# Kernel optimization log

Hardware: AMD Instinct MI355X
Metric: run time of the kernel (lower is better)

The kernel has to match this reference:

```python
import jax, jax.numpy as jnp
import numpy as np

K = 7        # kernel_size
G = 16       # group_number
STRIDE = 1
BN_EPS = 1e-5


def setup_inputs() -> dict:
    key = jax.random.key(0)
    ks = jax.random.split(key, 3)
    B, C, H, W = 2, 256, 56, 56
    Cr = C // 4  # reduction_ratio = 4
    x = jax.random.normal(ks[0], (B, C, H, W), dtype=jnp.float32)
    w1 = jax.random.normal(ks[1], (Cr, C), dtype=jnp.float32) * (1.0 / np.sqrt(C))
    b1 = jnp.zeros((Cr,), dtype=jnp.float32)
    gamma = jnp.ones((Cr,), dtype=jnp.float32)
    beta = jnp.zeros((Cr,), dtype=jnp.float32)
    w2 = jax.random.normal(ks[2], (K * K * G, Cr), dtype=jnp.float32) * (1.0 / np.sqrt(Cr))
    b2 = jnp.zeros((K * K * G,), dtype=jnp.float32)
    return {"x": x, "w1": w1, "b1": b1, "gamma": gamma, "beta": beta, "w2": w2, "b2": b2}


def _kernel_gen(x, w1, b1, gamma, beta, w2, b2):
    # 1x1 conv -> BatchNorm (training-mode batch stats) -> ReLU -> 1x1 conv
    t = jnp.einsum('oc,bchw->bohw', w1, x) + b1[None, :, None, None]
    mean = t.mean(axis=(0, 2, 3), keepdims=True)
    var = t.var(axis=(0, 2, 3), keepdims=True)
    t = (t - mean) * jax.lax.rsqrt(var + BN_EPS)
    t = t * gamma[None, :, None, None] + beta[None, :, None, None]
    t = jax.nn.relu(t)
    return jnp.einsum('oc,bchw->bohw', w2, t) + b2[None, :, None, None]


def reference(x, w1, b1, gamma, beta, w2, b2):
    B, C, H, W = x.shape
    nh, nw = H // STRIDE, W // STRIDE  # stride == 1 here
    # kernel generation (stride==1 -> no avg_pool)
    k = _kernel_gen(x, w1, b1, gamma, beta, w2, b2)          # (B, K*K*G, nh, nw)
    kernel = k.reshape(B, K * K, nh, nw, G)                   # raw view, as in torch
    # F.unfold with padding=K//2, stride=1 -> layout (B, C*K*K, L), c-major then k
    p = K // 2
    xp = jnp.pad(x, ((0, 0), (0, 0), (p, p), (p, p)))
    patches = jnp.stack(
        [xp[:, :, i:i + nh, j:j + nw] for i in range(K) for j in range(K)],
        axis=2)                                               # (B, C, K*K, nh, nw)
    flat = patches.reshape(B, C * K * K, nh * nw)             # == torch F.unfold
    ip = flat.reshape(B, C // G, K * K, nh, nw, G)            # raw view, as in torch
    out = (kernel[:, None] * ip).sum(axis=2)                  # (B, C//G, nh, nw, G)
    out = out.reshape(B, C, nh, nw)                           # raw view, as in torch
    return out, kernel
```

## Files before the change

### kernel.cpp

```cpp
#include <hip/hip_runtime.h>

#define HW     3136
#define C_IN   256
#define CR     64
#define KKG    784
#define NB     2
#define NPIX   6272
#define NT25   25
#define BN_EPS 1e-5f

__device__ float g_P[4 * CR * NPIX];
__device__ float g_T[CR * NPIX];
__device__ float g_bs[2 * CR * NT25];
__device__ float g_ss[2 * CR];
__device__ float g_xg[16 * NPIX * 16];

__global__ __launch_bounds__(256) void k1a_conv1(const float* __restrict__ x,
                                                 const float* __restrict__ w1) {
  int p = blockIdx.x * 256 + threadIdx.x;
  if (p >= NPIX) return;
  int o0 = blockIdx.y * 4;
  int kc = blockIdx.z;
  int b  = p / HW;
  int u  = p - b * HW;

  const float* xb = x + ((size_t)(b * C_IN + kc * 64)) * HW + u;
  const float* w  = w1 + kc * 64;

  float a0 = 0.f, a1 = 0.f, a2 = 0.f, a3 = 0.f;
#pragma unroll 8
  for (int c = 0; c < 64; ++c) {
    float xv = xb[(size_t)c * HW];
    a0 += w[(o0 + 0) * C_IN + c] * xv;
    a1 += w[(o0 + 1) * C_IN + c] * xv;
    a2 += w[(o0 + 2) * C_IN + c] * xv;
    a3 += w[(o0 + 3) * C_IN + c] * xv;
  }
  float* pp = g_P + ((size_t)kc * CR + o0) * NPIX + p;
  pp[0 * NPIX] = a0; pp[1 * NPIX] = a1; pp[2 * NPIX] = a2; pp[3 * NPIX] = a3;
}

__global__ __launch_bounds__(256) void k1b_reduce(const float* __restrict__ b1) {
  int p = blockIdx.x * 256 + threadIdx.x;
  int o = blockIdx.y;
  bool valid = (p < NPIX);
  float v = 0.0f;
  if (valid) {
    v = b1[o]
      + g_P[((size_t)0 * CR + o) * NPIX + p]
      + g_P[((size_t)1 * CR + o) * NPIX + p]
      + g_P[((size_t)2 * CR + o) * NPIX + p]
      + g_P[((size_t)3 * CR + o) * NPIX + p];
    g_T[(size_t)o * NPIX + p] = v;
  }
  float s  = valid ? v : 0.0f;
  float s2 = valid ? v * v : 0.0f;
#pragma unroll
  for (int off = 32; off > 0; off >>= 1) {
    s  += __shfl_down(s, off);
    s2 += __shfl_down(s2, off);
  }
  __shared__ float sd[8];
  int lane = threadIdx.x & 63, wid = threadIdx.x >> 6;
  if (lane == 0) { sd[wid] = s; sd[4 + wid] = s2; }
  __syncthreads();
  if (threadIdx.x == 0) {
    g_bs[o * NT25 + blockIdx.x]             = sd[0] + sd[1] + sd[2] + sd[3];
    g_bs[CR * NT25 + o * NT25 + blockIdx.x] = sd[4] + sd[5] + sd[6] + sd[7];
  }
}

__global__ __launch_bounds__(256) void k0t_transpose(const float* __restrict__ x,
                                                     const float* __restrict__ gamma,
                                                     const float* __restrict__ beta) {
  int d = blockIdx.x;
  int p = blockIdx.y * 256 + threadIdx.x;
  if (p < NPIX) {
    int b  = (p >= HW) ? 1 : 0;
    int hw = p - b * HW;
    const float* xp = x + ((size_t)(b * C_IN + d)) * HW + hw;
    float r[16];
#pragma unroll
    for (int cg = 0; cg < 16; ++cg)
      r[cg] = xp[(size_t)cg * (16 * HW)];
    float4* dst = (float4*)(g_xg + (((size_t)d * NPIX + p) << 4));
    dst[0] = make_float4(r[0], r[1], r[2], r[3]);
    dst[1] = make_float4(r[4], r[5], r[6], r[7]);
    dst[2] = make_float4(r[8], r[9], r[10], r[11]);
    dst[3] = make_float4(r[12], r[13], r[14], r[15]);
  }
  if (blockIdx.x == 0 && blockIdx.y == 0 && threadIdx.x < CR) {
    int o = threadIdx.x;
    float S = 0.f, S2 = 0.f;
#pragma unroll
    for (int px = 0; px < NT25; ++px) {
      S  += g_bs[o * NT25 + px];
      S2 += g_bs[CR * NT25 + o * NT25 + px];
    }
    const float invN = 1.0f / (float)NPIX;
    float mean = S * invN;
    float var  = S2 * invN - mean * mean;
    float inv  = rsqrtf(var + BN_EPS);
    float sc   = gamma[o] * inv;
    g_ss[o]      = sc;
    g_ss[CR + o] = beta[o] - mean * sc;
  }
}

__global__ __launch_bounds__(256) void k3_conv2(const float* __restrict__ w2,
                                                const float* __restrict__ b2,
                                                float* __restrict__ kout) {
  __shared__ float ssc[CR], ssh[CR];
  if (threadIdx.x < 2 * CR) {
    float v = g_ss[threadIdx.x];
    if (threadIdx.x < CR) ssc[threadIdx.x] = v; else ssh[threadIdx.x - CR] = v;
  }
  __syncthreads();

  int l  = blockIdx.x * 256 + threadIdx.x;
  if (l >= HW) return;
  int o0 = blockIdx.y * 16;
  int b  = blockIdx.z;

  float acc[16];
#pragma unroll
  for (int i = 0; i < 16; ++i) acc[i] = b2[o0 + i];

  const float* Tb = g_T + (size_t)b * HW + l;
  const float* w  = w2 + (size_t)o0 * CR;
#pragma unroll 4
  for (int c = 0; c < CR; ++c) {
    float tv = Tb[(size_t)c * NPIX];
    tv = fmaxf(tv * ssc[c] + ssh[c], 0.0f);
#pragma unroll
    for (int i = 0; i < 16; ++i)
      acc[i] += w[i * CR + c] * tv;
  }
  float* kb = kout + (size_t)(b * KKG + o0) * HW + l;
#pragma unroll
  for (int i = 0; i < 16; ++i) kb[(size_t)i * HW] = acc[i];
}

__global__ __launch_bounds__(256) void k4_invol(const float* __restrict__ kout,
                                                float* __restrict__ out) {
  int base = blockIdx.x * 256 + threadIdx.x;
  int b    = blockIdx.y;
  int cg0  = blockIdx.z * 8;

  int s = base / HW;
  int u = base - s * HW;
  int yrow = u / 56;
  int yy0 = yrow - 3;
  int xx0 = (u - yrow * 56) - 3;

  const float* kb = kout + (size_t)b * (KKG * HW) + base;

  float acc[8];
#pragma unroll
  for (int i = 0; i < 8; ++i) acc[i] = 0.0f;

#pragma unroll 7
  for (int kk = 0; kk < 49; ++kk) {
    int t16 = 16 * kk + s;
    int d   = t16 / 49;
    int kkp = t16 - d * 49;
    int ki  = kkp / 7;
    int kj  = kkp - ki * 7;
    int yy = yy0 + ki, xx = xx0 + kj;
    float kv = kb[(size_t)kk * 50176];
    int off;
    if ((unsigned)yy < 56u && (unsigned)xx < 56u) {
      off = yy * 56 + xx;
    } else {
      off = 0;
      kv = 0.0f;
    }
    const float* xp = g_xg + ((((size_t)d * NPIX + b * HW + off) << 4) + cg0);
    float4 xa = *(const float4*)xp;
    float4 xb4 = *(const float4*)(xp + 4);
    acc[0] += kv * xa.x;  acc[1] += kv * xa.y;
    acc[2] += kv * xa.z;  acc[3] += kv * xa.w;
    acc[4] += kv * xb4.x; acc[5] += kv * xb4.y;
    acc[6] += kv * xb4.z; acc[7] += kv * xb4.w;
  }

  float* ob = out + (size_t)b * (C_IN * HW) + (size_t)cg0 * 50176 + base;
#pragma unroll
  for (int cg = 0; cg < 8; ++cg) ob[(size_t)cg * 50176] = acc[cg];
}

extern "C" void kernel_launch(void* const* d_in, const int* in_sizes, int n_in,
                              void* d_out, int out_size, void* d_ws, size_t ws_size,
                              hipStream_t stream) {
  const float* x     = (const float*)d_in[0];
  const float* w1    = (const float*)d_in[1];
  const float* b1    = (const float*)d_in[2];
  const float* gamma = (const float*)d_in[3];
  const float* beta  = (const float*)d_in[4];
  const float* w2    = (const float*)d_in[5];
  const float* b2    = (const float*)d_in[6];

  float* out  = (float*)d_out;
  float* kout = out + (size_t)NB * C_IN * HW;

  k1a_conv1<<<dim3(25, 16, 4), 256, 0, stream>>>(x, w1);
  k1b_reduce<<<dim3(25, CR), 256, 0, stream>>>(b1);
  k0t_transpose<<<dim3(16, NT25), 256, 0, stream>>>(x, gamma, beta);
  k3_conv2<<<dim3(13, 49, NB), 256, 0, stream>>>(w2, b2, kout);
  k4_invol<<<dim3(196, NB, 2), 256, 0, stream>>>(kout, out);
}
```

Measured before the change: 141.4 us.

## Merge reduce and transpose kernels, fold BN finalize into conv2, regrid involution

Merges the bias-sum/statistics reduction and the x transpose into one launch that picks its role from blockIdx.y. The BN scale/shift finalization moves into every conv2 block, so the g_ss global round trip and the serial single-block step go away. The involution kernel is regridded so each block row maps to one s slice (13x16x4 grid), which removes per-thread division and pads 3136 up to 3328 threads per slice. Together these cut one kernel launch, though every conv2 block now recomputes the BN statistics redundantly.

```diff
diff --git a/kernel.cpp b/kernel.cpp
--- a/kernel.cpp
+++ b/kernel.cpp
@@ -12,7 +12,6 @@
 __device__ float g_P[4 * CR * NPIX];
 __device__ float g_T[CR * NPIX];
 __device__ float g_bs[2 * CR * NT25];
-__device__ float g_ss[2 * CR];
 __device__ float g_xg[16 * NPIX * 16];
 
 __global__ __launch_bounds__(256) void k1a_conv1(const float* __restrict__ x,
@@ -40,42 +39,39 @@
   pp[0 * NPIX] = a0; pp[1 * NPIX] = a1; pp[2 * NPIX] = a2; pp[3 * NPIX] = a3;
 }
 
-__global__ __launch_bounds__(256) void k1b_reduce(const float* __restrict__ b1) {
+__global__ __launch_bounds__(256) void kRT(const float* __restrict__ x,
+                                           const float* __restrict__ b1) {
   int p = blockIdx.x * 256 + threadIdx.x;
-  int o = blockIdx.y;
-  bool valid = (p < NPIX);
-  float v = 0.0f;
-  if (valid) {
-    v = b1[o]
-      + g_P[((size_t)0 * CR + o) * NPIX + p]
-      + g_P[((size_t)1 * CR + o) * NPIX + p]
-      + g_P[((size_t)2 * CR + o) * NPIX + p]
-      + g_P[((size_t)3 * CR + o) * NPIX + p];
-    g_T[(size_t)o * NPIX + p] = v;
-  }
-  float s  = valid ? v : 0.0f;
-  float s2 = valid ? v * v : 0.0f;
-#pragma unroll
-  for (int off = 32; off > 0; off >>= 1) {
-    s  += __shfl_down(s, off);
-    s2 += __shfl_down(s2, off);
-  }
-  __shared__ float sd[8];
-  int lane = threadIdx.x & 63, wid = threadIdx.x >> 6;
-  if (lane == 0) { sd[wid] = s; sd[4 + wid] = s2; }
-  __syncthreads();
-  if (threadIdx.x == 0) {
-    g_bs[o * NT25 + blockIdx.x]             = sd[0] + sd[1] + sd[2] + sd[3];
-    g_bs[CR * NT25 + o * NT25 + blockIdx.x] = sd[4] + sd[5] + sd[6] + sd[7];
-  }
-}
-
-__global__ __launch_bounds__(256) void k0t_transpose(const float* __restrict__ x,
-                                                     const float* __restrict__ gamma,
-                                                     const float* __restrict__ beta) {
-  int d = blockIdx.x;
-  int p = blockIdx.y * 256 + threadIdx.x;
-  if (p < NPIX) {
+  if (blockIdx.y < 64) {
+    int o = blockIdx.y;
+    bool valid = (p < NPIX);
+    float v = 0.0f;
+    if (valid) {
+      v = b1[o]
+        + g_P[((size_t)0 * CR + o) * NPIX + p]
+        + g_P[((size_t)1 * CR + o) * NPIX + p]
+        + g_P[((size_t)2 * CR + o) * NPIX + p]
+        + g_P[((size_t)3 * CR + o) * NPIX + p];
+      g_T[(size_t)o * NPIX + p] = v;
+    }
+    float s  = valid ? v : 0.0f;
+    float s2 = valid ? v * v : 0.0f;
+#pragma unroll
+    for (int off = 32; off > 0; off >>= 1) {
+      s  += __shfl_down(s, off);
+      s2 += __shfl_down(s2, off);
+    }
+    __shared__ float sd[8];
+    int lane = threadIdx.x & 63, wid = threadIdx.x >> 6;
+    if (lane == 0) { sd[wid] = s; sd[4 + wid] = s2; }
+    __syncthreads();
+    if (threadIdx.x == 0) {
+      g_bs[o * NT25 + blockIdx.x]             = sd[0] + sd[1] + sd[2] + sd[3];
+      g_bs[CR * NT25 + o * NT25 + blockIdx.x] = sd[4] + sd[5] + sd[6] + sd[7];
+    }
+  } else {
+    int d = blockIdx.y - 64;
+    if (p >= NPIX) return;
     int b  = (p >= HW) ? 1 : 0;
     int hw = p - b * HW;
     const float* xp = x + ((size_t)(b * C_IN + d)) * HW + hw;
@@ -89,7 +85,15 @@
     dst[2] = make_float4(r[8], r[9], r[10], r[11]);
     dst[3] = make_float4(r[12], r[13], r[14], r[15]);
   }
-  if (blockIdx.x == 0 && blockIdx.y == 0 && threadIdx.x < CR) {
+}
+
+__global__ __launch_bounds__(256) void k3_conv2(const float* __restrict__ gamma,
+                                                const float* __restrict__ beta,
+                                                const float* __restrict__ w2,
+                                                const float* __restrict__ b2,
+                                                float* __restrict__ kout) {
+  __shared__ float ssc[CR], ssh[CR];
+  if (threadIdx.x < CR) {
     int o = threadIdx.x;
     float S = 0.f, S2 = 0.f;
 #pragma unroll
@@ -102,18 +106,8 @@
     float var  = S2 * invN - mean * mean;
     float inv  = rsqrtf(var + BN_EPS);
     float sc   = gamma[o] * inv;
-    g_ss[o]      = sc;
-    g_ss[CR + o] = beta[o] - mean * sc;
-  }
-}
-
-__global__ __launch_bounds__(256) void k3_conv2(const float* __restrict__ w2,
-                                                const float* __restrict__ b2,
-                                                float* __restrict__ kout) {
-  __shared__ float ssc[CR], ssh[CR];
-  if (threadIdx.x < 2 * CR) {
-    float v = g_ss[threadIdx.x];
-    if (threadIdx.x < CR) ssc[threadIdx.x] = v; else ssh[threadIdx.x - CR] = v;
+    ssc[o] = sc;
+    ssh[o] = beta[o] - mean * sc;
   }
   __syncthreads();
 
@@ -143,17 +137,19 @@
 
 __global__ __launch_bounds__(256) void k4_invol(const float* __restrict__ kout,
                                                 float* __restrict__ out) {
-  int base = blockIdx.x * 256 + threadIdx.x;
-  int b    = blockIdx.y;
-  int cg0  = blockIdx.z * 8;
-
-  int s = base / HW;
-  int u = base - s * HW;
+  int u = blockIdx.x * 256 + threadIdx.x;
+  if (u >= HW) return;
+  int s   = blockIdx.y;
+  int bz  = blockIdx.z;
+  int b   = bz >> 1;
+  int cg0 = (bz & 1) * 8;
+
   int yrow = u / 56;
-  int yy0 = yrow - 3;
-  int xx0 = (u - yrow * 56) - 3;
-
-  const float* kb = kout + (size_t)b * (KKG * HW) + base;
+  int col  = u - yrow * 56;
+
+  const float* kb = kout + (size_t)b * (KKG * HW) + (size_t)s * HW + u;
+  const float* xg = g_xg + cg0;
+  const size_t bHW16 = (size_t)(b * HW) << 4;
 
   float acc[8];
 #pragma unroll
@@ -166,8 +162,8 @@
     int kkp = t16 - d * 49;
     int ki  = kkp / 7;
     int kj  = kkp - ki * 7;
-    int yy = yy0 + ki, xx = xx0 + kj;
-    float kv = kb[(size_t)kk * 50176];
+    int yy = yrow + ki - 3, xx = col + kj - 3;
+    float kv = kb[(size_t)kk * (16 * HW)];
     int off;
     if ((unsigned)yy < 56u && (unsigned)xx < 56u) {
       off = yy * 56 + xx;
@@ -175,8 +171,8 @@
       off = 0;
       kv = 0.0f;
     }
-    const float* xp = g_xg + ((((size_t)d * NPIX + b * HW + off) << 4) + cg0);
-    float4 xa = *(const float4*)xp;
+    const float* xp = xg + (((size_t)d * NPIX + off) << 4) + bHW16;
+    float4 xa  = *(const float4*)xp;
     float4 xb4 = *(const float4*)(xp + 4);
     acc[0] += kv * xa.x;  acc[1] += kv * xa.y;
     acc[2] += kv * xa.z;  acc[3] += kv * xa.w;
@@ -184,9 +180,9 @@
     acc[6] += kv * xb4.z; acc[7] += kv * xb4.w;
   }
 
-  float* ob = out + (size_t)b * (C_IN * HW) + (size_t)cg0 * 50176 + base;
-#pragma unroll
-  for (int cg = 0; cg < 8; ++cg) ob[(size_t)cg * 50176] = acc[cg];
+  float* ob = out + (size_t)b * (C_IN * HW) + ((size_t)(16 * cg0 + s)) * HW + u;
+#pragma unroll
+  for (int cg = 0; cg < 8; ++cg) ob[(size_t)cg * (16 * HW)] = acc[cg];
 }
 
 extern "C" void kernel_launch(void* const* d_in, const int* in_sizes, int n_in,
@@ -204,8 +200,7 @@
   float* kout = out + (size_t)NB * C_IN * HW;
 
   k1a_conv1<<<dim3(25, 16, 4), 256, 0, stream>>>(x, w1);
-  k1b_reduce<<<dim3(25, CR), 256, 0, stream>>>(b1);
-  k0t_transpose<<<dim3(16, NT25), 256, 0, stream>>>(x, gamma, beta);
-  k3_conv2<<<dim3(13, 49, NB), 256, 0, stream>>>(w2, b2, kout);
-  k4_invol<<<dim3(196, NB, 2), 256, 0, stream>>>(kout, out);
-}
+  kRT<<<dim3(25, 80), 256, 0, stream>>>(x, b1);
+  k3_conv2<<<dim3(13, 49, NB), 256, 0, stream>>>(gamma, beta, w2, b2, kout);
+  k4_invol<<<dim3(13, 16, 4), 256, 0, stream>>>(kout, out);
+}
```

New measurement: 139.1 us. No clear change (-1.6%).
